# Kernel optimization log

Hardware: AMD Instinct MI355X
Metric: run time of the kernel (lower is better)

The kernel has to match this reference:

```python
import jax, jax.numpy as jnp
import numpy as np

B, C, O, N, T, K = 4, 64, 64, 32768, 4, 9
PAD, DIL = 4, 1  # padding*dilation, dilation
SIGMA = 0.05
EPS_BN = 1e-5


def _gather_ch(x, idx):
    # x: [B, C, N], idx: [B, N] -> gather along last dim per channel
    idx3 = jnp.broadcast_to(idx[:, None, :], x.shape)
    return jnp.take_along_axis(x, idx3, axis=-1)


def _weighted_conv(x, coords, w):
    # x: [B,C,N], coords: [B,3,N], w: [O,C,K]
    xp = jnp.pad(x, ((0, 0), (0, 0), (PAD, PAD)))
    cp = jnp.pad(coords, ((0, 0), (0, 0), (PAD, PAD)))
    win_idx = jnp.arange(N)[:, None] + jnp.arange(K) * DIL  # [N, K]
    win = xp[:, :, win_idx]   # [B,C,N,K]
    cwin = cp[:, :, win_idx]  # [B,3,N,K]
    d = cwin - cwin[:, :, :, K // 2:K // 2 + 1]
    s = jnp.sum(d * d, axis=1)                    # [B,N,K]
    r = jnp.sqrt(jnp.where(s > 0, s, 1.0))
    r = jnp.where(s > 0, r, 0.0)
    wgt = jnp.maximum(1.0 - r / SIGMA, 0.0)       # [B,N,K]
    return jnp.einsum('bcnk,bnk,ock->bon', win, wgt, w)


def _bn(x, g, b):
    # training-mode BatchNorm1d over (B, N)
    m = jnp.mean(x, axis=(0, 2), keepdims=True)
    v = jnp.var(x, axis=(0, 2), keepdims=True)
    return g[None, :, None] * (x - m) * jax.lax.rsqrt(v + EPS_BN) + b[None, :, None]


def setup_inputs() -> dict:
    key = jax.random.key(0)
    ks = jax.random.split(key, 12)
    inp = jax.random.normal(ks[0], (B, C, N), dtype=jnp.float32)
    # coords in a small box so sigma=0.05 yields non-trivial weights
    multi_coords = jax.random.uniform(ks[1], (B, 3, N, T), dtype=jnp.float32) * 0.02
    indices = jax.random.randint(ks[2], (B, N, T), 0, N, dtype=jnp.int32)
    reindices = jax.random.randint(ks[3], (B, N, T), 0, N, dtype=jnp.int32)
    fan = C * K
    conv_w = jax.random.normal(ks[4], (T, O, C, K), dtype=jnp.float32) / np.sqrt(fan)
    bn_gamma = jnp.ones((T, O), dtype=jnp.float32)
    bn_beta = jnp.zeros((T, O), dtype=jnp.float32)
    fusion_w = jax.random.normal(ks[5], (O, T * O), dtype=jnp.float32) / np.sqrt(T * O)
    fusion_b = jnp.zeros((O,), dtype=jnp.float32)
    fusion_gamma = jnp.ones((O,), dtype=jnp.float32)
    fusion_beta = jnp.zeros((O,), dtype=jnp.float32)
    return {"input": inp, "multi_coords": multi_coords, "indices": indices,
            "reindices": reindices, "conv_w": conv_w, "bn_gamma": bn_gamma,
            "bn_beta": bn_beta, "fusion_w": fusion_w, "fusion_b": fusion_b,
            "fusion_gamma": fusion_gamma, "fusion_beta": fusion_beta}


def reference(input, multi_coords, indices, reindices, conv_w, bn_gamma, bn_beta,
              fusion_w, fusion_b, fusion_gamma, fusion_beta):
    outs = []
    for i in range(T):  # fixed small set of 4 Hilbert orders
        x = _gather_ch(input, indices[:, :, i])            # [B,C,N]
        x = _weighted_conv(x, multi_coords[:, :, :, i], conv_w[i])  # [B,O,N]
        x = _bn(x, bn_gamma[i], bn_beta[i])
        x = _gather_ch(x, reindices[:, :, i])
        outs.append(x)
    cat = jnp.concatenate(outs, axis=1)                    # [B, T*O, N]
    y = jnp.einsum('bcn,oc->bon', cat, fusion_w) + fusion_b[None, :, None]
    y = _bn(y, fusion_gamma, fusion_beta)
    return jax.nn.relu(y)
```

## Files before the change

kernel.cpp:

```cpp
#include <hip/hip_runtime.h>
#include <hip/hip_bf16.h>

#define BB 4
#define CC 64
#define OO 64
#define NN 32768
#define TT 4
#define KK 9
#define PADW 4
#define SIGMA 0.05f
#define EPS_BN 1e-5f

typedef __attribute__((ext_vector_type(8))) short bf16x8;
typedef __attribute__((ext_vector_type(4))) float f32x4;

__device__ __forceinline__ unsigned short f2bf(float f) {
  __hip_bfloat16 h = __float2bfloat16(f);
  return *reinterpret_cast<unsigned short*>(&h);
}
__device__ __forceinline__ float bf2f(unsigned short u) {
  unsigned int x = ((unsigned int)u) << 16;
  float f;
  __builtin_memcpy(&f, &x, 4);
  return f;
}
__device__ __forceinline__ unsigned int pkbf(float a, float b) {
  float2 t; t.x = a; t.y = b;
  __hip_bfloat162 h = __float22bfloat162_rn(t);
  unsigned int r;
  __builtin_memcpy(&r, &h, 4);
  return r;
}

__global__ __launch_bounds__(256) void transpose_kernel(
    const float* __restrict__ inp, unsigned short* __restrict__ xTb)
{
  const int n0 = blockIdx.x * 64;
  const int b  = blockIdx.y;
  const int tid = threadIdx.x;
  __shared__ float xt[64][65];
  {
    int nl = tid & 63, c4 = tid >> 6;
    #pragma unroll
    for (int i = 0; i < 16; ++i) {
      int c = c4 * 16 + i;
      xt[c][nl] = inp[((size_t)(b*CC + c))*NN + n0 + nl];
    }
  }
  __syncthreads();
  {
    int nl = tid >> 2, cq = tid & 3;
    unsigned int pk[8];
    #pragma unroll
    for (int i = 0; i < 8; ++i) {
      int c = cq*16 + i*2;
      pk[i] = pkbf(xt[c][nl], xt[c+1][nl]);
    }
    unsigned int* dst = (unsigned int*)(xTb + (((size_t)b*NN) + n0 + nl)*CC + cq*16);
    ((int4*)dst)[0] = make_int4((int)pk[0],(int)pk[1],(int)pk[2],(int)pk[3]);
    ((int4*)dst)[1] = make_int4((int)pk[4],(int)pk[5],(int)pk[6],(int)pk[7]);
  }
}

__global__ __launch_bounds__(256) void wprep_kernel(
    const float* __restrict__ cw, unsigned short* __restrict__ W4)
{
  const int k = blockIdx.x;
  const int t = blockIdx.y;
  for (int u = threadIdx.x; u < OO*CC; u += 256) {
    int o = u >> 6, c = u & 63;
    int ow = o >> 5, ot = (o >> 4) & 1, l15 = o & 15;
    int frag = c >> 5, q = (c >> 3) & 3, j = c & 7;
    float wv = cw[(((size_t)(t*OO + o))*CC + c)*KK + k];
    W4[(size_t)(t*9+k)*4096 + ow*2048 + ot*1024 + frag*512 + l15*32 + q*8 + j]
        = f2bf(wv);
  }
}

__global__ __launch_bounds__(256, 4) void conv_kernel(
    const unsigned short* __restrict__ xTb,
    const float* __restrict__ mc,
    const int*   __restrict__ ind,
    const unsigned short* __restrict__ W4,
    unsigned short* __restrict__ Y,
    float* __restrict__ cpart2)
{
  const int n0  = blockIdx.x * 128;
  const int b   = blockIdx.y;
  const int t   = blockIdx.z;
  const int tid = threadIdx.x;
  const int lane = tid & 63;
  const int w    = tid >> 6;
  const int l15  = lane & 15;
  const int q    = lane >> 4;
  const int ow   = w & 1;
  const int nw   = w >> 1;

  __shared__ short xg[136][72];
  __shared__ float wgl[128][10];
  __shared__ float mcs[3][140];

  int4 g[5];
  #pragma unroll
  for (int i = 0; i < 5; ++i) {
    int u = tid + 256*i;
    g[i] = make_int4(0,0,0,0);
    if (u < 1088) {
      int p = u >> 3, s = u & 7;
      int m = n0 + p - PADW;
      if (m >= 0 && m < NN) {
        int idx = ind[((size_t)b*NN + m)*TT + t];
        g[i] = *(const int4*)(xTb + ((size_t)b*NN + idx)*CC + s*8);
      }
    }
  }

  if (tid < 136) {
    int m = n0 + tid - PADW;
    #pragma unroll
    for (int d = 0; d < 3; ++d) {
      float4 v = make_float4(0.f, 0.f, 0.f, 0.f);
      if (m >= 0 && m < NN)
        v = *(const float4*)(mc + (((size_t)(b*3+d))*NN + m)*TT);
      mcs[d][tid] = (t==0) ? v.x : (t==1) ? v.y : (t==2) ? v.z : v.w;
    }
  }

  #pragma unroll
  for (int i = 0; i < 5; ++i) {
    int u = tid + 256*i;
    if (u < 1088) {
      int p = u >> 3, s = u & 7;
      *(int4*)&xg[p][s*8] = g[i];
    }
  }
  __syncthreads();

  {
    int nl = tid >> 1;
    int k0 = (tid & 1) * 5;
    int kc = 5 - (tid & 1);
    float cx = mcs[0][nl+4], cy = mcs[1][nl+4], cz = mcs[2][nl+4];
    for (int i2 = 0; i2 < kc; ++i2) {
      int k = k0 + i2, mi = nl + k;
      float dx = mcs[0][mi]-cx, dy = mcs[1][mi]-cy, dz = mcs[2][mi]-cz;
      float s2 = dx*dx + dy*dy + dz*dz;
      float r = (s2 > 0.f) ? sqrtf(s2) : 0.f;
      wgl[nl][k] = fmaxf(1.f - r*(1.f/SIGMA), 0.f);
    }
  }
  __syncthreads();

  const unsigned short* Wt = W4 + (size_t)t*9*4096 + ow*2048 + (l15*4 + q)*8;
  const f32x4 Z = {0.f, 0.f, 0.f, 0.f};
  f32x4 fin[2][4];
  #pragma unroll
  for (int ot = 0; ot < 2; ++ot)
    #pragma unroll
    for (int ns = 0; ns < 4; ++ns) fin[ot][ns] = Z;

  for (int k = 0; k < KK; ++k) {
    const unsigned short* Wk = Wt + (size_t)k*4096;
    bf16x8 af[2][2];
    #pragma unroll
    for (int ot = 0; ot < 2; ++ot) {
      af[ot][0] = *(const bf16x8*)(Wk + ot*1024);
      af[ot][1] = *(const bf16x8*)(Wk + ot*1024 + 512);
    }
    #pragma unroll
    for (int ns = 0; ns < 4; ++ns) {
      int nl = nw*64 + ns*16 + l15;
      int p  = nl + k;
      bf16x8 b0 = *(const bf16x8*)&xg[p][q*8];
      bf16x8 b1 = *(const bf16x8*)&xg[p][32 + q*8];
      float wgt = wgl[nl][k];
      #pragma unroll
      for (int ot = 0; ot < 2; ++ot) {
        f32x4 d = __builtin_amdgcn_mfma_f32_16x16x32_bf16(af[ot][0], b0, Z, 0, 0, 0);
        d = __builtin_amdgcn_mfma_f32_16x16x32_bf16(af[ot][1], b1, d, 0, 0, 0);
        fin[ot][ns] += wgt * d;
      }
    }
  }

  #pragma unroll
  for (int ns = 0; ns < 4; ++ns) {
    int nl = nw*64 + ns*16 + l15;
    size_t row = (((size_t)t*BB + b)*NN + n0 + nl)*OO;
    #pragma unroll
    for (int ot = 0; ot < 2; ++ot) {
      uint2 pk2;
      pk2.x = pkbf(fin[ot][ns][0], fin[ot][ns][1]);
      pk2.y = pkbf(fin[ot][ns][2], fin[ot][ns][3]);
      *(uint2*)(Y + row + ow*32 + ot*16 + q*4) = pk2;
    }
  }

  float sv[16];
  #pragma unroll
  for (int ot = 0; ot < 2; ++ot)
    #pragma unroll
    for (int r = 0; r < 4; ++r) {
      float a = 0.f, qs = 0.f;
      #pragma unroll
      for (int ns = 0; ns < 4; ++ns) {
        float v = fin[ot][ns][r];
        a += v; qs += v*v;
      }
      sv[ot*4+r] = a; sv[8+ot*4+r] = qs;
    }
  #pragma unroll
  for (int msk = 1; msk < 16; msk <<= 1) {
    #pragma unroll
    for (int i = 0; i < 16; ++i) sv[i] += __shfl_xor(sv[i], msk, 16);
  }
  if (l15 == 0) {
    int slot4 = ((b*256 + (int)blockIdx.x) << 2) | w;
    #pragma unroll
    for (int ot = 0; ot < 2; ++ot)
      #pragma unroll
      for (int r = 0; r < 4; ++r) {
        int o = ow*32 + ot*16 + q*4 + r;
        cpart2[((size_t)((t*64 + o)*2 + 0))*4096 + slot4] = sv[ot*4+r];
        cpart2[((size_t)((t*64 + o)*2 + 1))*4096 + slot4] = sv[8+ot*4+r];
      }
  }
}

__global__ __launch_bounds__(256) void bnparam_kernel(
    const float* __restrict__ cpart2,
    const float* __restrict__ gam,
    const float* __restrict__ bet,
    float* __restrict__ ss)
{
  const int to = blockIdx.x;
  const int tid = threadIdx.x;
  __shared__ float r1[256], r2[256];
  const float* p1 = cpart2 + (size_t)to*2*4096;
  const float* p2 = p1 + 4096;
  float s1 = 0.f, s2 = 0.f;
  for (int i = tid*4; i < 4096; i += 1024) {
    float4 a = *(const float4*)(p1 + i);
    float4 c = *(const float4*)(p2 + i);
    s1 += a.x + a.y + a.z + a.w;
    s2 += c.x + c.y + c.z + c.w;
  }
  r1[tid] = s1; r2[tid] = s2;
  __syncthreads();
  for (int st = 128; st > 0; st >>= 1) {
    if (tid < st) { r1[tid] += r1[tid+st]; r2[tid] += r2[tid+st]; }
    __syncthreads();
  }
  if (tid == 0) {
    const float inv = 1.f / (float)(BB * NN);
    float mean = r1[0] * inv;
    float var  = r2[0] * inv - mean * mean;
    float sc = gam[to] * rsqrtf(var + EPS_BN);
    ss[to*2 + 0] = sc;
    ss[to*2 + 1] = bet[to] - mean * sc;
  }
}

__global__ __launch_bounds__(256, 4) void fusion_kernel(
    const unsigned short* __restrict__ Y,
    const int*   __restrict__ rind,
    const float* __restrict__ ss,
    const float* __restrict__ fw,
    const float* __restrict__ fb,
    float* __restrict__ out)
{
  const int n0  = blockIdx.x * 128;
  const int b   = blockIdx.y;
  const int tid = threadIdx.x;
  const int lane = tid & 63;
  const int w    = tid >> 6;
  const int l15  = lane & 15;
  const int q    = lane >> 4;
  const int ow   = w & 1;
  const int nw   = w >> 1;

  __shared__ short zg[128][72];
  __shared__ int   rnl[TT][128];
  __shared__ float ssl[512];

  for (int u = tid; u < 512; u += 256) {
    int tt = u >> 7, nl = u & 127;
    rnl[tt][nl] = rind[((size_t)b*NN + n0 + nl)*TT + tt];
  }
  ssl[tid]       = ss[tid];
  ssl[tid + 256] = ss[tid + 256];
  __syncthreads();

  f32x4 fin[2][4];
  #pragma unroll
  for (int ot = 0; ot < 2; ++ot)
    #pragma unroll
    for (int ns = 0; ns < 4; ++ns) fin[ot][ns] = (f32x4){0.f,0.f,0.f,0.f};

  for (int r = 0; r < 4; ++r) {
    if (r) __syncthreads();
    #pragma unroll
    for (int i = 0; i < 4; ++i) {
      int u = tid + 256*i;
      int n = u >> 3, s = u & 7;
      int rn = rnl[r][n];
      int4 raw = *(const int4*)(Y + (((size_t)r*BB + b)*NN + rn)*OO + s*8);
      const unsigned short* rp = (const unsigned short*)&raw;
      int cb = r*64 + s*8;
      unsigned int pk[4];
      #pragma unroll
      for (int j = 0; j < 4; ++j) {
        float v0 = bf2f(rp[2*j  ]) * ssl[(cb+2*j  )*2] + ssl[(cb+2*j  )*2+1];
        float v1 = bf2f(rp[2*j+1]) * ssl[(cb+2*j+1)*2] + ssl[(cb+2*j+1)*2+1];
        pk[j] = pkbf(v0, v1);
      }
      *(int4*)&zg[n][s*8] = make_int4((int)pk[0],(int)pk[1],(int)pk[2],(int)pk[3]);
    }
    __syncthreads();

    #pragma unroll
    for (int kk = 0; kk < 2; ++kk) {
      bf16x8 af[2];
      #pragma unroll
      for (int ot = 0; ot < 2; ++ot) {
        const float* wp = fw + (size_t)(ow*32 + ot*16 + l15)*256 + r*64 + kk*32 + q*8;
        float4 wa = *(const float4*)wp;
        float4 wb = *(const float4*)(wp + 4);
        unsigned int u0 = pkbf(wa.x, wa.y), u1 = pkbf(wa.z, wa.w);
        unsigned int u2 = pkbf(wb.x, wb.y), u3 = pkbf(wb.z, wb.w);
        int4 tmp = make_int4((int)u0,(int)u1,(int)u2,(int)u3);
        __builtin_memcpy(&af[ot], &tmp, 16);
      }
      #pragma unroll
      for (int ns = 0; ns < 4; ++ns) {
        int nl = nw*64 + ns*16 + l15;
        bf16x8 bfr = *(const bf16x8*)&zg[nl][kk*32 + q*8];
        #pragma unroll
        for (int ot = 0; ot < 2; ++ot)
          fin[ot][ns] = __builtin_amdgcn_mfma_f32_16x16x32_bf16(af[ot], bfr, fin[ot][ns], 0, 0, 0);
      }
    }
  }

  #pragma unroll
  for (int ot = 0; ot < 2; ++ot)
    #pragma unroll
    for (int rr = 0; rr < 4; ++rr) {
      int o = ow*32 + ot*16 + q*4 + rr;
      float bias = fb[o];
      float* dst = out + ((size_t)(b*OO + o))*NN + n0 + nw*64;
      #pragma unroll
      for (int ns = 0; ns < 4; ++ns)
        dst[ns*16 + l15] = fin[ot][ns][rr] + bias;
    }
}

__global__ __launch_bounds__(256) void fstat_kernel(
    const float* __restrict__ out, float* __restrict__ fpart)
{
  const int o = blockIdx.x, b = blockIdx.y;
  const int tid = threadIdx.x;
  __shared__ float r1[256], r2[256];
  const float* src = out + ((size_t)(b*OO + o))*NN;
  float s1 = 0.f, s2 = 0.f;
  for (int i = tid*4; i < NN; i += 1024) {
    float4 v = *(const float4*)(src + i);
    s1 += v.x + v.y + v.z + v.w;
    s2 += v.x*v.x + v.y*v.y + v.z*v.z + v.w*v.w;
  }
  r1[tid] = s1; r2[tid] = s2;
  __syncthreads();
  for (int st = 128; st > 0; st >>= 1) {
    if (tid < st) { r1[tid] += r1[tid+st]; r2[tid] += r2[tid+st]; }
    __syncthreads();
  }
  if (tid == 0) {
    fpart[(b*OO + o)*2 + 0] = r1[0];
    fpart[(b*OO + o)*2 + 1] = r2[0];
  }
}

__global__ void freduce_kernel(
    const float* __restrict__ fpart,
    const float* __restrict__ fg,
    const float* __restrict__ fbeta,
    float* __restrict__ fss)
{
  int o = threadIdx.x;
  float s1 = 0.f, s2 = 0.f;
  #pragma unroll
  for (int b = 0; b < BB; ++b) {
    s1 += fpart[(b*OO + o)*2 + 0];
    s2 += fpart[(b*OO + o)*2 + 1];
  }
  const float inv = 1.f / (float)(BB * NN);
  float mean = s1 * inv;
  float var  = s2 * inv - mean * mean;
  float sc = fg[o] * rsqrtf(var + EPS_BN);
  fss[o*2 + 0] = sc;
  fss[o*2 + 1] = fbeta[o] - mean * sc;
}

__global__ __launch_bounds__(256) void final_kernel(
    float* __restrict__ out, const float* __restrict__ fss)
{
  const int e0 = blockIdx.x * 2048 + threadIdx.x;
  #pragma unroll
  for (int s = 0; s < 8; ++s) {
    int e  = e0 + s * 256;
    int o2 = (e >> 15) & 63;
    float sc = fss[o2*2 + 0];
    float sh = fss[o2*2 + 1];
    float v = out[e] * sc + sh;
    out[e] = fmaxf(v, 0.f);
  }
}

extern "C" void kernel_launch(void* const* d_in, const int* in_sizes, int n_in,
                              void* d_out, int out_size, void* d_ws, size_t ws_size,
                              hipStream_t stream) {
  const float* inp  = (const float*)d_in[0];
  const float* mc   = (const float*)d_in[1];
  const int*   ind  = (const int*)  d_in[2];
  const int*   rind = (const int*)  d_in[3];
  const float* cw   = (const float*)d_in[4];
  const float* bg   = (const float*)d_in[5];
  const float* bb   = (const float*)d_in[6];
  const float* fw   = (const float*)d_in[7];
  const float* fb   = (const float*)d_in[8];
  const float* fg   = (const float*)d_in[9];
  const float* fbt  = (const float*)d_in[10];

  char* ws = (char*)d_ws;
  float* convss = (float*)(ws + 0);
  float* fss    = (float*)(ws + 2048);
  float* fpart  = (float*)(ws + 2560);
  unsigned short* Y = (unsigned short*)(ws + 8192);

  char* ob = (char*)d_out;
  unsigned short* xTb = (unsigned short*)ob;
  unsigned short* W4  = (unsigned short*)(ob + 16777216);
  float*          cpart2 = (float*)(ob + 17072128);
  float* out = (float*)d_out;

  dim3 gt(NN/64, BB);
  transpose_kernel<<<gt, 256, 0, stream>>>(inp, xTb);

  dim3 gw(KK, TT);
  wprep_kernel<<<gw, 256, 0, stream>>>(cw, W4);

  dim3 gc(NN/128, BB, TT);
  conv_kernel<<<gc, 256, 0, stream>>>(xTb, mc, ind, W4, Y, cpart2);

  bnparam_kernel<<<256, 256, 0, stream>>>(cpart2, bg, bb, convss);

  dim3 gf(NN/128, BB);
  fusion_kernel<<<gf, 256, 0, stream>>>(Y, rind, convss, fw, fb, out);

  dim3 gs(OO, BB);
  fstat_kernel<<<gs, 256, 0, stream>>>(out, fpart);

  freduce_kernel<<<1, 64, 0, stream>>>(fpart, fg, fbt, fss);

  final_kernel<<<(BB*OO*NN)/2048, 256, 0, stream>>>(out, fss);
}
```

Baseline: 239.3 us.

## Loop over Hilbert orders inside conv kernel and prefetch next gather

The conv kernel no longer launches one block per order t. Each block now loops over all four orders, loading coordinates and indices for every order once into shared memory. While the MFMAs for order t run, the gathered input rows for order t+1 are prefetched into registers. This hides the irregular gather latency behind compute and removes redundant coordinate and index loads, at the cost of a grid four times smaller, an extra barrier per iteration and higher register pressure.

```diff
diff --git a/kernel.cpp b/kernel.cpp
--- a/kernel.cpp
+++ b/kernel.cpp
@@ -87,7 +87,6 @@
 {
   const int n0  = blockIdx.x * 128;
   const int b   = blockIdx.y;
-  const int t   = blockIdx.z;
   const int tid = threadIdx.x;
   const int lane = tid & 63;
   const int w    = tid >> 6;
@@ -98,7 +97,8 @@
 
   __shared__ short xg[136][72];
   __shared__ float wgl[128][10];
-  __shared__ float mcs[3][140];
+  __shared__ float mcs[3][4][140];
+  __shared__ int   indl[136][4];
 
   int4 g[5];
   #pragma unroll
@@ -109,7 +109,7 @@
       int p = u >> 3, s = u & 7;
       int m = n0 + p - PADW;
       if (m >= 0 && m < NN) {
-        int idx = ind[((size_t)b*NN + m)*TT + t];
+        int idx = ind[((size_t)b*NN + m)*TT + 0];
         g[i] = *(const int4*)(xTb + ((size_t)b*NN + idx)*CC + s*8);
       }
     }
@@ -117,12 +117,17 @@
 
   if (tid < 136) {
     int m = n0 + tid - PADW;
+    int4 iv = make_int4(0,0,0,0);
+    if (m >= 0 && m < NN)
+      iv = *(const int4*)(ind + ((size_t)b*NN + m)*TT);
+    *(int4*)&indl[tid][0] = iv;
     #pragma unroll
     for (int d = 0; d < 3; ++d) {
       float4 v = make_float4(0.f, 0.f, 0.f, 0.f);
       if (m >= 0 && m < NN)
         v = *(const float4*)(mc + (((size_t)(b*3+d))*NN + m)*TT);
-      mcs[d][tid] = (t==0) ? v.x : (t==1) ? v.y : (t==2) ? v.z : v.w;
+      mcs[d][0][tid] = v.x; mcs[d][1][tid] = v.y;
+      mcs[d][2][tid] = v.z; mcs[d][3][tid] = v.w;
     }
   }
 
@@ -136,94 +141,126 @@
   }
   __syncthreads();
 
-  {
-    int nl = tid >> 1;
-    int k0 = (tid & 1) * 5;
-    int kc = 5 - (tid & 1);
-    float cx = mcs[0][nl+4], cy = mcs[1][nl+4], cz = mcs[2][nl+4];
-    for (int i2 = 0; i2 < kc; ++i2) {
-      int k = k0 + i2, mi = nl + k;
-      float dx = mcs[0][mi]-cx, dy = mcs[1][mi]-cy, dz = mcs[2][mi]-cz;
-      float s2 = dx*dx + dy*dy + dz*dz;
-      float r = (s2 > 0.f) ? sqrtf(s2) : 0.f;
-      wgl[nl][k] = fmaxf(1.f - r*(1.f/SIGMA), 0.f);
-    }
-  }
-  __syncthreads();
-
-  const unsigned short* Wt = W4 + (size_t)t*9*4096 + ow*2048 + (l15*4 + q)*8;
-  const f32x4 Z = {0.f, 0.f, 0.f, 0.f};
-  f32x4 fin[2][4];
-  #pragma unroll
-  for (int ot = 0; ot < 2; ++ot)
-    #pragma unroll
-    for (int ns = 0; ns < 4; ++ns) fin[ot][ns] = Z;
-
-  for (int k = 0; k < KK; ++k) {
-    const unsigned short* Wk = Wt + (size_t)k*4096;
-    bf16x8 af[2][2];
-    #pragma unroll
-    for (int ot = 0; ot < 2; ++ot) {
-      af[ot][0] = *(const bf16x8*)(Wk + ot*1024);
-      af[ot][1] = *(const bf16x8*)(Wk + ot*1024 + 512);
-    }
+  for (int t = 0; t < TT; ++t) {
+    {
+      int nl = tid >> 1;
+      int k0 = (tid & 1) * 5;
+      int kc = 5 - (tid & 1);
+      float cx = mcs[0][t][nl+4], cy = mcs[1][t][nl+4], cz = mcs[2][t][nl+4];
+      for (int i2 = 0; i2 < kc; ++i2) {
+        int k = k0 + i2, mi = nl + k;
+        float dx = mcs[0][t][mi]-cx, dy = mcs[1][t][mi]-cy, dz = mcs[2][t][mi]-cz;
+        float s2 = dx*dx + dy*dy + dz*dz;
+        float r = (s2 > 0.f) ? sqrtf(s2) : 0.f;
+        wgl[nl][k] = fmaxf(1.f - r*(1.f/SIGMA), 0.f);
+      }
+    }
+
+    if (t < TT-1) {
+      #pragma unroll
+      for (int i = 0; i < 5; ++i) {
+        int u = tid + 256*i;
+        g[i] = make_int4(0,0,0,0);
+        if (u < 1088) {
+          int p = u >> 3, s = u & 7;
+          int m = n0 + p - PADW;
+          if (m >= 0 && m < NN) {
+            int idx = indl[p][t+1];
+            g[i] = *(const int4*)(xTb + ((size_t)b*NN + idx)*CC + s*8);
+          }
+        }
+      }
+    }
+    __syncthreads();
+
+    const unsigned short* Wt = W4 + (size_t)t*9*4096 + ow*2048 + (l15*4 + q)*8;
+    const f32x4 Z = {0.f, 0.f, 0.f, 0.f};
+    f32x4 fin[2][4];
+    #pragma unroll
+    for (int ot = 0; ot < 2; ++ot)
+      #pragma unroll
+      for (int ns = 0; ns < 4; ++ns) fin[ot][ns] = Z;
+
+    for (int k = 0; k < KK; ++k) {
+      const unsigned short* Wk = Wt + (size_t)k*4096;
+      bf16x8 af[2][2];
+      #pragma unroll
+      for (int ot = 0; ot < 2; ++ot) {
+        af[ot][0] = *(const bf16x8*)(Wk + ot*1024);
+        af[ot][1] = *(const bf16x8*)(Wk + ot*1024 + 512);
+      }
+      #pragma unroll
+      for (int ns = 0; ns < 4; ++ns) {
+        int nl = nw*64 + ns*16 + l15;
+        int p  = nl + k;
+        bf16x8 b0 = *(const bf16x8*)&xg[p][q*8];
+        bf16x8 b1 = *(const bf16x8*)&xg[p][32 + q*8];
+        float wgt = wgl[nl][k];
+        #pragma unroll
+        for (int ot = 0; ot < 2; ++ot) {
+          f32x4 d = __builtin_amdgcn_mfma_f32_16x16x32_bf16(af[ot][0], b0, Z, 0, 0, 0);
+          d = __builtin_amdgcn_mfma_f32_16x16x32_bf16(af[ot][1], b1, d, 0, 0, 0);
+          fin[ot][ns] += wgt * d;
+        }
+      }
+    }
+
     #pragma unroll
     for (int ns = 0; ns < 4; ++ns) {
       int nl = nw*64 + ns*16 + l15;
-      int p  = nl + k;
-      bf16x8 b0 = *(const bf16x8*)&xg[p][q*8];
-      bf16x8 b1 = *(const bf16x8*)&xg[p][32 + q*8];
-      float wgt = wgl[nl][k];
+      size_t row = (((size_t)t*BB + b)*NN + n0 + nl)*OO;
       #pragma unroll
       for (int ot = 0; ot < 2; ++ot) {
-        f32x4 d = __builtin_amdgcn_mfma_f32_16x16x32_bf16(af[ot][0], b0, Z, 0, 0, 0);
-        d = __builtin_amdgcn_mfma_f32_16x16x32_bf16(af[ot][1], b1, d, 0, 0, 0);
-        fin[ot][ns] += wgt * d;
-      }
-    }
-  }
-
-  #pragma unroll
-  for (int ns = 0; ns < 4; ++ns) {
-    int nl = nw*64 + ns*16 + l15;
-    size_t row = (((size_t)t*BB + b)*NN + n0 + nl)*OO;
-    #pragma unroll
-    for (int ot = 0; ot < 2; ++ot) {
-      uint2 pk2;
-      pk2.x = pkbf(fin[ot][ns][0], fin[ot][ns][1]);
-      pk2.y = pkbf(fin[ot][ns][2], fin[ot][ns][3]);
-      *(uint2*)(Y + row + ow*32 + ot*16 + q*4) = pk2;
-    }
-  }
-
-  float sv[16];
-  #pragma unroll
-  for (int ot = 0; ot < 2; ++ot)
-    #pragma unroll
-    for (int r = 0; r < 4; ++r) {
-      float a = 0.f, qs = 0.f;
-      #pragma unroll
-      for (int ns = 0; ns < 4; ++ns) {
-        float v = fin[ot][ns][r];
-        a += v; qs += v*v;
-      }
-      sv[ot*4+r] = a; sv[8+ot*4+r] = qs;
-    }
-  #pragma unroll
-  for (int msk = 1; msk < 16; msk <<= 1) {
-    #pragma unroll
-    for (int i = 0; i < 16; ++i) sv[i] += __shfl_xor(sv[i], msk, 16);
-  }
-  if (l15 == 0) {
-    int slot4 = ((b*256 + (int)blockIdx.x) << 2) | w;
-    #pragma unroll
-    for (int ot = 0; ot < 2; ++ot)
-      #pragma unroll
-      for (int r = 0; r < 4; ++r) {
-        int o = ow*32 + ot*16 + q*4 + r;
-        cpart2[((size_t)((t*64 + o)*2 + 0))*4096 + slot4] = sv[ot*4+r];
-        cpart2[((size_t)((t*64 + o)*2 + 1))*4096 + slot4] = sv[8+ot*4+r];
-      }
+        uint2 pk2;
+        pk2.x = pkbf(fin[ot][ns][0], fin[ot][ns][1]);
+        pk2.y = pkbf(fin[ot][ns][2], fin[ot][ns][3]);
+        *(uint2*)(Y + row + ow*32 + ot*16 + q*4) = pk2;
+      }
+    }
+
+    {
+      float sv[16];
+      #pragma unroll
+      for (int ot = 0; ot < 2; ++ot)
+        #pragma unroll
+        for (int r = 0; r < 4; ++r) {
+          float a = 0.f, qs = 0.f;
+          #pragma unroll
+          for (int ns = 0; ns < 4; ++ns) {
+            float v = fin[ot][ns][r];
+            a += v; qs += v*v;
+          }
+          sv[ot*4+r] = a; sv[8+ot*4+r] = qs;
+        }
+      #pragma unroll
+      for (int msk = 1; msk < 16; msk <<= 1) {
+        #pragma unroll
+        for (int i = 0; i < 16; ++i) sv[i] += __shfl_xor(sv[i], msk, 16);
+      }
+      if (l15 == 0) {
+        int slot4 = ((b*256 + (int)blockIdx.x) << 2) | w;
+        #pragma unroll
+        for (int ot = 0; ot < 2; ++ot)
+          #pragma unroll
+          for (int r = 0; r < 4; ++r) {
+            int o = ow*32 + ot*16 + q*4 + r;
+            cpart2[((size_t)((t*64 + o)*2 + 0))*4096 + slot4] = sv[ot*4+r];
+            cpart2[((size_t)((t*64 + o)*2 + 1))*4096 + slot4] = sv[8+ot*4+r];
+          }
+      }
+    }
+
+    if (t < TT-1) {
+      __syncthreads();
+      #pragma unroll
+      for (int i = 0; i < 5; ++i) {
+        int u = tid + 256*i;
+        if (u < 1088) {
+          int p = u >> 3, s = u & 7;
+          *(int4*)&xg[p][s*8] = g[i];
+        }
+      }
+    }
   }
 }
 
@@ -449,7 +486,7 @@
   dim3 gw(KK, TT);
   wprep_kernel<<<gw, 256, 0, stream>>>(cw, W4);
 
-  dim3 gc(NN/128, BB, TT);
+  dim3 gc(NN/128, BB);
   conv_kernel<<<gc, 256, 0, stream>>>(xTb, mc, ind, W4, Y, cpart2);
 
   bnparam_kernel<<<256, 256, 0, stream>>>(cpart2, bg, bb, convss);
```

Measured after the change: 245.1 us. 2.4% more time.

## Fold conv BN into fusion weights, fuse output stats, swizzle LDS tiles

Applied to the files above, without the earlier changes.

The per-channel conv BatchNorm scale is folded into the fusion weights and its shift into a precomputed bias, so the fusion kernel copies raw gathered bf16 rows into LDS with no per-element affine. The separate fstat pass over the whole output is removed: fusion computes per-channel sum and sum-of-squares in registers, reduces them with shuffles and atomically adds them into a zeroed partial buffer. Both LDS tiles change from padded rows to an XOR-swizzled layout to avoid bank conflicts without padding, and the conv gather splits index loading from data loading to expose more memory-level parallelism. Risks are atomic contention on 128 floats and a different bf16 rounding point, since the scale is now applied to the weights rather than the activations.

```diff
diff --git a/kernel.cpp b/kernel.cpp
--- a/kernel.cpp
+++ b/kernel.cpp
@@ -96,23 +96,28 @@
   const int ow   = w & 1;
   const int nw   = w >> 1;
 
-  __shared__ short xg[136][72];
+  __shared__ short xg[136*64];
   __shared__ float wgl[128][10];
   __shared__ float mcs[3][140];
 
-  int4 g[5];
+  int idxr[5];
   #pragma unroll
   for (int i = 0; i < 5; ++i) {
     int u = tid + 256*i;
+    int p = u >> 3;
+    int m = n0 + p - PADW;
+    idxr[i] = -1;
+    if (u < 1088 && m >= 0 && m < NN)
+      idxr[i] = ind[((size_t)b*NN + m)*TT + t];
+  }
+
+  int4 g[5];
+  #pragma unroll
+  for (int i = 0; i < 5; ++i) {
+    int s = (tid + 256*i) & 7;
     g[i] = make_int4(0,0,0,0);
-    if (u < 1088) {
-      int p = u >> 3, s = u & 7;
-      int m = n0 + p - PADW;
-      if (m >= 0 && m < NN) {
-        int idx = ind[((size_t)b*NN + m)*TT + t];
-        g[i] = *(const int4*)(xTb + ((size_t)b*NN + idx)*CC + s*8);
-      }
-    }
+    if (idxr[i] >= 0)
+      g[i] = *(const int4*)(xTb + ((size_t)b*NN + idxr[i])*CC + s*8);
   }
 
   if (tid < 136) {
@@ -131,7 +136,7 @@
     int u = tid + 256*i;
     if (u < 1088) {
       int p = u >> 3, s = u & 7;
-      *(int4*)&xg[p][s*8] = g[i];
+      *(int4*)&xg[(p << 6) + ((s ^ (p & 7)) << 3)] = g[i];
     }
   }
   __syncthreads();
@@ -171,8 +176,10 @@
     for (int ns = 0; ns < 4; ++ns) {
       int nl = nw*64 + ns*16 + l15;
       int p  = nl + k;
-      bf16x8 b0 = *(const bf16x8*)&xg[p][q*8];
-      bf16x8 b1 = *(const bf16x8*)&xg[p][32 + q*8];
+      const short* row = &xg[p << 6];
+      int sw = p & 7;
+      bf16x8 b0 = *(const bf16x8*)(row + ((q ^ sw) << 3));
+      bf16x8 b1 = *(const bf16x8*)(row + (((4 + q) ^ sw) << 3));
       float wgt = wgl[nl][k];
       #pragma unroll
       for (int ot = 0; ot < 2; ++ot) {
@@ -261,13 +268,32 @@
   }
 }
 
+__global__ __launch_bounds__(256) void wfuse_kernel(
+    const float* __restrict__ fw,
+    const float* __restrict__ fb,
+    const float* __restrict__ ss,
+    float* __restrict__ fbp,
+    float* __restrict__ fpart)
+{
+  const int tid = threadIdx.x;
+  if (tid < 128) fpart[tid] = 0.f;
+  int o = tid >> 2, c0 = (tid & 3) * 64;
+  float s = 0.f;
+  for (int c = c0; c < c0 + 64; ++c)
+    s += fw[o*256 + c] * ss[c*2 + 1];
+  s += __shfl_xor(s, 1);
+  s += __shfl_xor(s, 2);
+  if ((tid & 3) == 0) fbp[o] = fb[o] + s;
+}
+
 __global__ __launch_bounds__(256, 4) void fusion_kernel(
     const unsigned short* __restrict__ Y,
     const int*   __restrict__ rind,
     const float* __restrict__ ss,
     const float* __restrict__ fw,
-    const float* __restrict__ fb,
-    float* __restrict__ out)
+    const float* __restrict__ fbp,
+    float* __restrict__ out,
+    float* __restrict__ fpart)
 {
   const int n0  = blockIdx.x * 128;
   const int b   = blockIdx.y;
@@ -279,17 +305,17 @@
   const int ow   = w & 1;
   const int nw   = w >> 1;
 
-  __shared__ short zg[128][72];
-  __shared__ int   rnl[TT][128];
-  __shared__ float ssl[512];
-
-  for (int u = tid; u < 512; u += 256) {
-    int tt = u >> 7, nl = u & 127;
-    rnl[tt][nl] = rind[((size_t)b*NN + n0 + nl)*TT + tt];
-  }
-  ssl[tid]       = ss[tid];
-  ssl[tid + 256] = ss[tid + 256];
-  __syncthreads();
+  __shared__ short zg[128*64];
+  __shared__ float scl[256];
+
+  scl[tid] = ss[tid*2];
+
+  int4 rg[4];
+  #pragma unroll
+  for (int i = 0; i < 4; ++i) {
+    int n = (tid >> 3) + 32*i;
+    rg[i] = *(const int4*)(rind + ((size_t)b*NN + n0 + n)*TT);
+  }
 
   f32x4 fin[2][4];
   #pragma unroll
@@ -297,24 +323,17 @@
     #pragma unroll
     for (int ns = 0; ns < 4; ++ns) fin[ot][ns] = (f32x4){0.f,0.f,0.f,0.f};
 
+  #pragma unroll
   for (int r = 0; r < 4; ++r) {
     if (r) __syncthreads();
     #pragma unroll
     for (int i = 0; i < 4; ++i) {
       int u = tid + 256*i;
       int n = u >> 3, s = u & 7;
-      int rn = rnl[r][n];
+      int rn = (r == 0) ? rg[i].x : (r == 1) ? rg[i].y
+             : (r == 2) ? rg[i].z : rg[i].w;
       int4 raw = *(const int4*)(Y + (((size_t)r*BB + b)*NN + rn)*OO + s*8);
-      const unsigned short* rp = (const unsigned short*)&raw;
-      int cb = r*64 + s*8;
-      unsigned int pk[4];
-      #pragma unroll
-      for (int j = 0; j < 4; ++j) {
-        float v0 = bf2f(rp[2*j  ]) * ssl[(cb+2*j  )*2] + ssl[(cb+2*j  )*2+1];
-        float v1 = bf2f(rp[2*j+1]) * ssl[(cb+2*j+1)*2] + ssl[(cb+2*j+1)*2+1];
-        pk[j] = pkbf(v0, v1);
-      }
-      *(int4*)&zg[n][s*8] = make_int4((int)pk[0],(int)pk[1],(int)pk[2],(int)pk[3]);
+      *(int4*)&zg[(n << 6) + ((s ^ (n & 7)) << 3)] = raw;
     }
     __syncthreads();
 
@@ -323,18 +342,23 @@
       bf16x8 af[2];
       #pragma unroll
       for (int ot = 0; ot < 2; ++ot) {
-        const float* wp = fw + (size_t)(ow*32 + ot*16 + l15)*256 + r*64 + kk*32 + q*8;
+        int o = ow*32 + ot*16 + l15;
+        int cb = r*64 + kk*32 + q*8;
+        const float* wp = fw + (size_t)o*256 + cb;
         float4 wa = *(const float4*)wp;
         float4 wb = *(const float4*)(wp + 4);
-        unsigned int u0 = pkbf(wa.x, wa.y), u1 = pkbf(wa.z, wa.w);
-        unsigned int u2 = pkbf(wb.x, wb.y), u3 = pkbf(wb.z, wb.w);
+        unsigned int u0 = pkbf(wa.x*scl[cb+0], wa.y*scl[cb+1]);
+        unsigned int u1 = pkbf(wa.z*scl[cb+2], wa.w*scl[cb+3]);
+        unsigned int u2 = pkbf(wb.x*scl[cb+4], wb.y*scl[cb+5]);
+        unsigned int u3 = pkbf(wb.z*scl[cb+6], wb.w*scl[cb+7]);
         int4 tmp = make_int4((int)u0,(int)u1,(int)u2,(int)u3);
         __builtin_memcpy(&af[ot], &tmp, 16);
       }
       #pragma unroll
       for (int ns = 0; ns < 4; ++ns) {
         int nl = nw*64 + ns*16 + l15;
-        bf16x8 bfr = *(const bf16x8*)&zg[nl][kk*32 + q*8];
+        int ch = (kk*4 + q) ^ (nl & 7);
+        bf16x8 bfr = *(const bf16x8*)&zg[(nl << 6) + (ch << 3)];
         #pragma unroll
         for (int ot = 0; ot < 2; ++ot)
           fin[ot][ns] = __builtin_amdgcn_mfma_f32_16x16x32_bf16(af[ot], bfr, fin[ot][ns], 0, 0, 0);
@@ -342,41 +366,37 @@
     }
   }
 
+  float sv[16];
   #pragma unroll
   for (int ot = 0; ot < 2; ++ot)
     #pragma unroll
-    for (int rr = 0; rr < 4; ++rr) {
-      int o = ow*32 + ot*16 + q*4 + rr;
-      float bias = fb[o];
+    for (int r2 = 0; r2 < 4; ++r2) {
+      int o = ow*32 + ot*16 + q*4 + r2;
+      float bias = fbp[o];
       float* dst = out + ((size_t)(b*OO + o))*NN + n0 + nw*64;
-      #pragma unroll
-      for (int ns = 0; ns < 4; ++ns)
-        dst[ns*16 + l15] = fin[ot][ns][rr] + bias;
-    }
-}
-
-__global__ __launch_bounds__(256) void fstat_kernel(
-    const float* __restrict__ out, float* __restrict__ fpart)
-{
-  const int o = blockIdx.x, b = blockIdx.y;
-  const int tid = threadIdx.x;
-  __shared__ float r1[256], r2[256];
-  const float* src = out + ((size_t)(b*OO + o))*NN;
-  float s1 = 0.f, s2 = 0.f;
-  for (int i = tid*4; i < NN; i += 1024) {
-    float4 v = *(const float4*)(src + i);
-    s1 += v.x + v.y + v.z + v.w;
-    s2 += v.x*v.x + v.y*v.y + v.z*v.z + v.w*v.w;
-  }
-  r1[tid] = s1; r2[tid] = s2;
-  __syncthreads();
-  for (int st = 128; st > 0; st >>= 1) {
-    if (tid < st) { r1[tid] += r1[tid+st]; r2[tid] += r2[tid+st]; }
-    __syncthreads();
-  }
-  if (tid == 0) {
-    fpart[(b*OO + o)*2 + 0] = r1[0];
-    fpart[(b*OO + o)*2 + 1] = r2[0];
+      float a = 0.f, qs = 0.f;
+      #pragma unroll
+      for (int ns = 0; ns < 4; ++ns) {
+        float v = fin[ot][ns][r2] + bias;
+        dst[ns*16 + l15] = v;
+        a += v; qs += v*v;
+      }
+      sv[ot*4+r2] = a; sv[8+ot*4+r2] = qs;
+    }
+  #pragma unroll
+  for (int msk = 1; msk < 16; msk <<= 1) {
+    #pragma unroll
+    for (int i = 0; i < 16; ++i) sv[i] += __shfl_xor(sv[i], msk, 16);
+  }
+  if (l15 == 0) {
+    #pragma unroll
+    for (int ot = 0; ot < 2; ++ot)
+      #pragma unroll
+      for (int r2 = 0; r2 < 4; ++r2) {
+        int o = ow*32 + ot*16 + q*4 + r2;
+        atomicAdd(&fpart[o*2 + 0], sv[ot*4+r2]);
+        atomicAdd(&fpart[o*2 + 1], sv[8+ot*4+r2]);
+      }
   }
 }
 
@@ -387,12 +407,8 @@
     float* __restrict__ fss)
 {
   int o = threadIdx.x;
-  float s1 = 0.f, s2 = 0.f;
-  #pragma unroll
-  for (int b = 0; b < BB; ++b) {
-    s1 += fpart[(b*OO + o)*2 + 0];
-    s2 += fpart[(b*OO + o)*2 + 1];
-  }
+  float s1 = fpart[o*2 + 0];
+  float s2 = fpart[o*2 + 1];
   const float inv = 1.f / (float)(BB * NN);
   float mean = s1 * inv;
   float var  = s2 * inv - mean * mean;
@@ -435,6 +451,7 @@
   float* convss = (float*)(ws + 0);
   float* fss    = (float*)(ws + 2048);
   float* fpart  = (float*)(ws + 2560);
+  float* fbp    = (float*)(ws + 3072);
   unsigned short* Y = (unsigned short*)(ws + 8192);
 
   char* ob = (char*)d_out;
@@ -454,11 +471,10 @@
 
   bnparam_kernel<<<256, 256, 0, stream>>>(cpart2, bg, bb, convss);
 
+  wfuse_kernel<<<1, 256, 0, stream>>>(fw, fb, convss, fbp, fpart);
+
   dim3 gf(NN/128, BB);
-  fusion_kernel<<<gf, 256, 0, stream>>>(Y, rind, convss, fw, fb, out);
-
-  dim3 gs(OO, BB);
-  fstat_kernel<<<gs, 256, 0, stream>>>(out, fpart);
+  fusion_kernel<<<gf, 256, 0, stream>>>(Y, rind, convss, fw, fbp, out, fpart);
 
   freduce_kernel<<<1, 64, 0, stream>>>(fpart, fg, fbt, fss);
 
```

New measurement: 623.6 us. 2.61x slower.
